# Kernel tuning notes

Hardware: AMD Instinct MI355X
Metric: run time of the kernel (lower is better)

## Reference

```python
import jax, jax.numpy as jnp
import numpy as np
import math

HEADS = 16


def setup_inputs() -> dict:
    key = jax.random.key(0)
    kx, kq, kk, kv = jax.random.split(key, 4)
    B, S, E = 2, 2048, 1024
    x = jax.random.normal(kx, (B, S, E), dtype=jnp.float32)
    # torch nn.Linear weights are [out, in]; y = x @ W.T
    Wq = jax.random.normal(kq, (E, E), dtype=jnp.float32) * (1.0 / math.sqrt(E))
    Wk = jax.random.normal(kk, (E, E), dtype=jnp.float32) * (1.0 / math.sqrt(E))
    Wv = jax.random.normal(kv, (E, E), dtype=jnp.float32) * (1.0 / math.sqrt(E))
    # multiplicative causal mask, as the module applies mask by elementwise multiply
    mask = jnp.tril(jnp.ones((S, S), dtype=jnp.float32))
    return {"x": x, "Wq": Wq, "Wk": Wk, "Wv": Wv, "mask": mask}


def reference(x, Wq, Wk, Wv, mask):
    B, S, E = x.shape
    H = HEADS
    D = E // H
    q = (x @ Wq.T).reshape(B, S, H, D)
    k = (x @ Wk.T).reshape(B, S, H, D)
    v = (x @ Wv.T).reshape(B, S, H, D)
    # scores: [B, H, S, S]
    sim = jnp.einsum('nqhd,nkhd->nhqk', q, k)
    sim = sim * mask  # multiplicative mask, broadcast over (B, H)
    # NOTE: original scales by sqrt(emsize), not sqrt(head_dim)
    attn = jax.nn.softmax(sim / math.sqrt(E), axis=-1)
    out = jnp.einsum('nhql,nlhd->nqhd', attn, v).reshape(B, S, E)
    return out
```

## Files before the change

kernel.cpp:

```cpp
#include <hip/hip_runtime.h>
#include <hip/hip_bf16.h>
#include <cstdint>

using bf16   = __bf16;
using bf16x4 = __attribute__((ext_vector_type(4))) __bf16;
using bf16x8 = __attribute__((ext_vector_type(8))) __bf16;
using f32x4  = __attribute__((ext_vector_type(4))) float;

#define MFMA16(a, b, c) __builtin_amdgcn_mfma_f32_16x16x32_bf16((a), (b), (c), 0, 0, 0)

__device__ __forceinline__ void load_lds16(const bf16* g, bf16* l) {
    __builtin_amdgcn_global_load_lds(
        (const __attribute__((address_space(1))) void*)g,
        (__attribute__((address_space(3))) void*)l, 16, 0, 0);
}

__global__ __launch_bounds__(256) void cast_all(const float* __restrict__ x,
                                                const float* __restrict__ Wq,
                                                const float* __restrict__ Wk,
                                                const float* __restrict__ Wv,
                                                bf16* __restrict__ xb,
                                                bf16* __restrict__ wb,
                                                float qscale) {
    int i = blockIdx.x * 256 + threadIdx.x;
    const float* src; bf16* dst; int off; float scale = 1.0f;
    if (i < 1048576)      { src = x;  dst = xb;              off = i; }
    else if (i < 1310720) { src = Wq; dst = wb;              off = i - 1048576; scale = qscale; }
    else if (i < 1572864) { src = Wk; dst = wb + (1u << 20); off = i - 1310720; }
    else                  { src = Wv; dst = wb + (2u << 20); off = i - 1572864; }
    float4 v = reinterpret_cast<const float4*>(src)[off];
    bf16x4 o;
    o[0] = (bf16)(v.x * scale); o[1] = (bf16)(v.y * scale);
    o[2] = (bf16)(v.z * scale); o[3] = (bf16)(v.w * scale);
    reinterpret_cast<bf16x4*>(dst)[off] = o;
}

__global__ __launch_bounds__(256) void qkv_gemm(const bf16* __restrict__ xb,
                                                const bf16* __restrict__ wb,
                                                bf16* __restrict__ Qo,
                                                bf16* __restrict__ Ko,
                                                bf16* __restrict__ Vt) {
    const int id  = blockIdx.x;
    const int xcd = id & 7;
    const int r   = id >> 3;
    const int ntile = r >> 2;
    const int ms    = r & 3;
    const int mtile = xcd * 4 + ms;
    const int n0 = ntile * 128;
    const int m0 = mtile * 128;

    __shared__ __align__(16) bf16 As[128 * 64];
    __shared__ __align__(16) bf16 Bs[128 * 64];

    const int t    = threadIdx.x;
    const int lane = t & 63;
    const int wid  = t >> 6;
    const int quad = lane >> 4;
    const int col  = lane & 15;
    const int wm   = wid & 1;
    const int wn   = wid >> 1;

    const int rsub = lane >> 3;
    const int csw  = ((lane & 7) ^ rsub) * 8;

    f32x4 acc[4][4] = {};

    const bf16* Ag = &xb[(size_t)(m0 + rsub) * 1024 + csw];
    const bf16* Bg = &wb[(size_t)(n0 + rsub) * 1024 + csw];

    for (int kc = 0; kc < 1024; kc += 64) {
        __syncthreads();
#pragma unroll
        for (int j = 0; j < 4; ++j) {
            const int c = wid * 4 + j;
            load_lds16(Ag + kc + (size_t)c * 8 * 1024, &As[c * 512]);
        }
#pragma unroll
        for (int j = 0; j < 4; ++j) {
            const int c = wid * 4 + j;
            load_lds16(Bg + kc + (size_t)c * 8 * 1024, &Bs[c * 512]);
        }
        __syncthreads();

#pragma unroll
        for (int ks = 0; ks < 2; ++ks) {
            const int ca = ((ks * 4 + quad) ^ (col & 7)) * 8;
            bf16x8 a[4], b[4];
#pragma unroll
            for (int i = 0; i < 4; ++i)
                a[i] = *reinterpret_cast<const bf16x8*>(
                    &As[(wm * 64 + i * 16 + col) * 64 + ca]);
#pragma unroll
            for (int i = 0; i < 4; ++i)
                b[i] = *reinterpret_cast<const bf16x8*>(
                    &Bs[(wn * 64 + i * 16 + col) * 64 + ca]);
#pragma unroll
            for (int mt = 0; mt < 4; ++mt)
#pragma unroll
                for (int nt = 0; nt < 4; ++nt)
                    acc[mt][nt] = MFMA16(a[mt], b[nt], acc[mt][nt]);
        }
    }

    const int w = ntile >> 3;
#pragma unroll
    for (int mt = 0; mt < 4; ++mt) {
#pragma unroll
        for (int nt = 0; nt < 4; ++nt) {
#pragma unroll
            for (int r2 = 0; r2 < 4; ++r2) {
                int m = m0 + wm * 64 + mt * 16 + quad * 4 + r2;
                int n = n0 + wn * 64 + nt * 16 + col;
                int bb = m >> 11, s = m & 2047;
                int n1 = n & 1023;
                int h = n1 >> 6, d = n1 & 63;
                size_t bh = (size_t)(bb * 16 + h);
                bf16 v = (bf16)acc[mt][nt][r2];
                if (w == 0)      Qo[(bh * 2048 + s) * 64 + d] = v;
                else if (w == 1) Ko[(bh * 2048 + s) * 64 + d] = v;
                else             Vt[(bh * 64 + d) * 2048 + s] = v;
            }
        }
    }
}

__global__ __launch_bounds__(256) void tail_kernel(const bf16* __restrict__ Vt,
                                                   float* __restrict__ Tail) {
    const int bh = blockIdx.x >> 3;
    const int dg = blockIdx.x & 7;
    const bf16* Vg = Vt + (size_t)bh * 64 * 2048 + (size_t)dg * 8 * 2048;
    float* Tg = Tail + (size_t)bh * 33 * 64 + dg * 8;

    __shared__ float ts[8 * 33];
    const int tid = threadIdx.x;
    const int d  = tid >> 5;
    const int tt = tid & 31;

    const bf16* p = &Vg[(size_t)d * 2048 + tt * 64];
    float s = 0.0f;
#pragma unroll
    for (int j = 0; j < 8; ++j) {
        bf16x8 v = *reinterpret_cast<const bf16x8*>(p + j * 8);
#pragma unroll
        for (int e = 0; e < 8; ++e) s += (float)v[e];
    }
    ts[d * 33 + tt] = s;
    __syncthreads();

    if (tid < 8) {
        const int dd = tid;
        float acc = 0.0f;
        Tg[32 * 64 + dd] = 0.0f;
        for (int t2 = 31; t2 >= 1; --t2) {
            acc += ts[dd * 33 + t2];
            Tg[t2 * 64 + dd] = acc;
        }
    }
}

__global__ __launch_bounds__(256) void attn_kernel(const bf16* __restrict__ Q,
                                                   const bf16* __restrict__ K,
                                                   const bf16* __restrict__ Vt,
                                                   const float* __restrict__ Tail,
                                                   float* __restrict__ out) {
    const int bid  = blockIdx.x;
    const int work = (bid & 7) * 64 + (bid >> 3);
    const int bh   = work >> 4;
    const int x    = work & 15;
    const int b    = bh >> 4;
    const int h    = bh & 15;

    const int t    = threadIdx.x;
    const int lane = t & 63;
    const int wid  = t >> 6;
    const int quad = lane >> 4;
    const int col  = lane & 15;
    const int qh   = wid & 1;
    const int kh   = wid >> 1;

    const bf16* Qg = Q + (size_t)bh * 2048 * 64;
    const bf16* Kg = K + (size_t)bh * 2048 * 64;
    const bf16* Vg = Vt + (size_t)bh * 64 * 2048;

    __shared__ __align__(16) bf16 Ks[128 * 64];
    __shared__ __align__(16) bf16 Vs[64 * 128];
    __shared__ __align__(16) bf16 Ps[64 * 136];

    bf16x8 ones;
#pragma unroll
    for (int i = 0; i < 8; ++i) ones[i] = (bf16)1.0f;

    const int rsubK = lane >> 3;
    const int cswK  = ((lane & 7) ^ rsubK) * 8;
    const int rV    = lane >> 4;
    const int ccV   = lane & 15;

    for (int pp = 0; pp < 2; ++pp) {
        const int qt = pp == 0 ? (31 - x) : x;
        const int q0 = qt * 64;
        const int np = (qt >> 1) + 1;

        bf16x8 qf[2][2];
#pragma unroll
        for (int qs = 0; qs < 2; ++qs)
#pragma unroll
            for (int ks = 0; ks < 2; ++ks)
                qf[qs][ks] = *reinterpret_cast<const bf16x8*>(
                    &Qg[(size_t)(q0 + qh * 32 + qs * 16 + col) * 64 + ks * 32 + quad * 8]);

        f32x4 o[2][2];
        f32x4 la[2];
        {
            const float tc = 64.0f * (float)(32 - 2 * np);
#pragma unroll
            for (int qs = 0; qs < 2; ++qs)
#pragma unroll
                for (int r = 0; r < 4; ++r) la[qs][r] = tc;
            const float* Tg = Tail + ((size_t)bh * 33 + 2 * np) * 64;
#pragma unroll
            for (int dt = 0; dt < 2; ++dt) {
                float tv = Tg[kh * 32 + dt * 16 + col];
#pragma unroll
                for (int qs = 0; qs < 2; ++qs)
#pragma unroll
                    for (int r = 0; r < 4; ++r) o[qs][dt][r] = tv;
            }
        }

        const int s0max = (np - 1) * 128;

        for (int s0 = 0; s0 < np * 128; s0 += 128) {
            __syncthreads();
#pragma unroll
            for (int jj = 0; jj < 4; ++jj) {
                const int c = wid * 4 + jj;
                load_lds16(&Kg[(size_t)(s0 + c * 8 + rsubK) * 64 + cswK], &Ks[c * 512]);
                const int d = c * 4 + rV;
                load_lds16(&Vg[(size_t)d * 2048 + s0 + ((ccV ^ (d & 15)) * 8)], &Vs[c * 512]);
            }
            __syncthreads();

            f32x4 sv[2][4] = {};
            __builtin_amdgcn_s_setprio(1);
#pragma unroll
            for (int ks = 0; ks < 2; ++ks) {
                const int ca = ((ks * 4 + quad) ^ (col & 7)) * 8;
#pragma unroll
                for (int nt = 0; nt < 4; ++nt) {
                    bf16x8 kb = *reinterpret_cast<const bf16x8*>(
                        &Ks[((kh * 4 + nt) * 16 + col) * 64 + ca]);
                    sv[0][nt] = MFMA16(kb, qf[0][ks], sv[0][nt]);
                    sv[1][nt] = MFMA16(kb, qf[1][ks], sv[1][nt]);
                }
            }
            __builtin_amdgcn_s_setprio(0);

            if (s0 == s0max) {
#pragma unroll
                for (int qs = 0; qs < 2; ++qs) {
                    const int qc = q0 + qh * 32 + qs * 16 + col;
#pragma unroll
                    for (int nt = 0; nt < 4; ++nt)
#pragma unroll
                        for (int r = 0; r < 4; ++r) {
                            int kidx = s0 + kh * 64 + nt * 16 + quad * 4 + r;
                            if (kidx > qc) sv[qs][nt][r] = 0.0f;
                        }
                }
            }

#pragma unroll
            for (int qs = 0; qs < 2; ++qs) {
                bf16* Pq = &Ps[(qh * 32 + qs * 16 + col) * 136 + kh * 64];
#pragma unroll
                for (int nt = 0; nt < 4; ++nt) {
                    bf16x4 pw;
#pragma unroll
                    for (int r = 0; r < 4; ++r)
                        pw[r] = (bf16)__builtin_amdgcn_exp2f(sv[qs][nt][r]);
                    *reinterpret_cast<bf16x4*>(&Pq[nt * 16 + quad * 4]) = pw;
                }
            }

            __syncthreads();

            __builtin_amdgcn_s_setprio(1);
#pragma unroll
            for (int kg = 0; kg < 4; ++kg) {
                bf16x8 pa0 = *reinterpret_cast<const bf16x8*>(
                    &Ps[(qh * 32 + col) * 136 + kg * 32 + quad * 8]);
                bf16x8 pa1 = *reinterpret_cast<const bf16x8*>(
                    &Ps[(qh * 32 + 16 + col) * 136 + kg * 32 + quad * 8]);
                la[0] = MFMA16(pa0, ones, la[0]);
                la[1] = MFMA16(pa1, ones, la[1]);
#pragma unroll
                for (int dt = 0; dt < 2; ++dt) {
                    bf16x8 vb = *reinterpret_cast<const bf16x8*>(
                        &Vs[(kh * 32 + dt * 16 + col) * 128 + ((kg * 4 + quad) ^ col) * 8]);
                    o[0][dt] = MFMA16(pa0, vb, o[0][dt]);
                    o[1][dt] = MFMA16(pa1, vb, o[1][dt]);
                }
            }
            __builtin_amdgcn_s_setprio(0);
        }

#pragma unroll
        for (int qs = 0; qs < 2; ++qs) {
#pragma unroll
            for (int r = 0; r < 4; ++r) {
                int q = q0 + qh * 32 + qs * 16 + quad * 4 + r;
                float inv = __builtin_amdgcn_rcpf(la[qs][r]);
#pragma unroll
                for (int dt = 0; dt < 2; ++dt) {
                    int d = kh * 32 + dt * 16 + col;
                    out[((size_t)b * 2048 + q) * 1024 + h * 64 + d] = o[qs][dt][r] * inv;
                }
            }
        }
    }
}

extern "C" void kernel_launch(void* const* d_in, const int* in_sizes, int n_in,
                              void* d_out, int out_size, void* d_ws, size_t ws_size,
                              hipStream_t stream) {
    const float* x  = (const float*)d_in[0];
    const float* Wq = (const float*)d_in[1];
    const float* Wk = (const float*)d_in[2];
    const float* Wv = (const float*)d_in[3];
    float* out = (float*)d_out;

    char* ws = (char*)d_ws;
    bf16*  xb   = (bf16*)(ws);
    bf16*  wb   = (bf16*)(ws + (size_t)(8  << 20));
    bf16*  Qb   = (bf16*)(ws + (size_t)(14 << 20));
    bf16*  Kb   = (bf16*)(ws + (size_t)(22 << 20));
    bf16*  Vtb  = (bf16*)(ws + (size_t)(30 << 20));
    float* Tail = (float*)(ws + (size_t)(38 << 20));

    const float QSCALE = 1.44269504088896f / 32.0f;

    cast_all<<<7168, 256, 0, stream>>>(x, Wq, Wk, Wv, xb, wb, QSCALE);

    qkv_gemm<<<768, 256, 0, stream>>>(xb, wb, Qb, Kb, Vtb);

    tail_kernel<<<256, 256, 0, stream>>>(Vtb, Tail);

    attn_kernel<<<512, 256, 0, stream>>>(Qb, Kb, Vtb, Tail, out);
}
```

Measured before the change: 157.6 us.

## Prefetch K/V tiles into registers and stage V-transpose stores through LDS

In the attention loop, the next K and V tiles are now loaded from global memory into registers during the PV MFMA phase, then written to LDS at the top of the next iteration. This replaces the direct global-to-LDS loads and is meant to hide global load latency behind compute. In the QKV GEMM, the V-transposed output is first written to shared memory and then stored as coalesced 16-byte rows, replacing scattered 2-byte strided stores. The cost is more register pressure from the prefetch buffers and extra LDS traffic plus synchronisation in the GEMM epilogue.

```diff
diff --git a/kernel.cpp b/kernel.cpp
--- a/kernel.cpp
+++ b/kernel.cpp
@@ -49,8 +49,9 @@
     const int n0 = ntile * 128;
     const int m0 = mtile * 128;
 
-    __shared__ __align__(16) bf16 As[128 * 64];
-    __shared__ __align__(16) bf16 Bs[128 * 64];
+    __shared__ __align__(16) bf16 SM[128 * 132];
+    bf16* const As = SM;
+    bf16* const Bs = SM + 128 * 64;
 
     const int t    = threadIdx.x;
     const int lane = t & 63;
@@ -103,22 +104,48 @@
     }
 
     const int w = ntile >> 3;
-#pragma unroll
-    for (int mt = 0; mt < 4; ++mt) {
-#pragma unroll
-        for (int nt = 0; nt < 4; ++nt) {
-#pragma unroll
-            for (int r2 = 0; r2 < 4; ++r2) {
-                int m = m0 + wm * 64 + mt * 16 + quad * 4 + r2;
-                int n = n0 + wn * 64 + nt * 16 + col;
-                int bb = m >> 11, s = m & 2047;
-                int n1 = n & 1023;
-                int h = n1 >> 6, d = n1 & 63;
-                size_t bh = (size_t)(bb * 16 + h);
-                bf16 v = (bf16)acc[mt][nt][r2];
-                if (w == 0)      Qo[(bh * 2048 + s) * 64 + d] = v;
-                else if (w == 1) Ko[(bh * 2048 + s) * 64 + d] = v;
-                else             Vt[(bh * 64 + d) * 2048 + s] = v;
+    if (w == 2) {
+        __syncthreads();
+#pragma unroll
+        for (int mt = 0; mt < 4; ++mt)
+#pragma unroll
+            for (int nt = 0; nt < 4; ++nt)
+#pragma unroll
+                for (int r2 = 0; r2 < 4; ++r2) {
+                    int s_local = wm * 64 + mt * 16 + quad * 4 + r2;
+                    int n_local = wn * 64 + nt * 16 + col;
+                    SM[n_local * 132 + s_local] = (bf16)acc[mt][nt][r2];
+                }
+        __syncthreads();
+        const int sbase = m0 & 2047;
+        const int bb16  = (m0 >> 11) * 16;
+#pragma unroll
+        for (int i = 0; i < 8; ++i) {
+            int task = i * 256 + t;
+            int row = task >> 4, ch = task & 15;
+            int n1 = (n0 + row) & 1023;
+            int hh = n1 >> 6, dd = n1 & 63;
+            bf16x8 v = *reinterpret_cast<const bf16x8*>(&SM[row * 132 + ch * 8]);
+            *reinterpret_cast<bf16x8*>(
+                &Vt[((size_t)(bb16 + hh) * 64 + dd) * 2048 + sbase + ch * 8]) = v;
+        }
+    } else {
+#pragma unroll
+        for (int mt = 0; mt < 4; ++mt) {
+#pragma unroll
+            for (int nt = 0; nt < 4; ++nt) {
+#pragma unroll
+                for (int r2 = 0; r2 < 4; ++r2) {
+                    int m = m0 + wm * 64 + mt * 16 + quad * 4 + r2;
+                    int n = n0 + wn * 64 + nt * 16 + col;
+                    int bb = m >> 11, s = m & 2047;
+                    int n1 = n & 1023;
+                    int h = n1 >> 6, d = n1 & 63;
+                    size_t bh = (size_t)(bb * 16 + h);
+                    bf16 v = (bf16)acc[mt][nt][r2];
+                    if (w == 0) Qo[(bh * 2048 + s) * 64 + d] = v;
+                    else        Ko[(bh * 2048 + s) * 64 + d] = v;
+                }
             }
         }
     }
@@ -229,14 +256,24 @@
 
         const int s0max = (np - 1) * 128;
 
-        for (int s0 = 0; s0 < np * 128; s0 += 128) {
+        float4 kr[4], vr[4];
+#pragma unroll
+        for (int jj = 0; jj < 4; ++jj) {
+            const int c = wid * 4 + jj;
+            kr[jj] = *reinterpret_cast<const float4*>(
+                &Kg[(size_t)(c * 8 + rsubK) * 64 + cswK]);
+            const int d = c * 4 + rV;
+            vr[jj] = *reinterpret_cast<const float4*>(
+                &Vg[(size_t)d * 2048 + ((ccV ^ (d & 15)) * 8)]);
+        }
+
+        for (int s0 = 0; s0 <= s0max; s0 += 128) {
             __syncthreads();
 #pragma unroll
             for (int jj = 0; jj < 4; ++jj) {
                 const int c = wid * 4 + jj;
-                load_lds16(&Kg[(size_t)(s0 + c * 8 + rsubK) * 64 + cswK], &Ks[c * 512]);
-                const int d = c * 4 + rV;
-                load_lds16(&Vg[(size_t)d * 2048 + s0 + ((ccV ^ (d & 15)) * 8)], &Vs[c * 512]);
+                *reinterpret_cast<float4*>(&Ks[c * 512 + lane * 8]) = kr[jj];
+                *reinterpret_cast<float4*>(&Vs[c * 512 + lane * 8]) = vr[jj];
             }
             __syncthreads();
 
@@ -283,6 +320,19 @@
             }
 
             __syncthreads();
+
+            if (s0 < s0max) {
+                const int s0n = s0 + 128;
+#pragma unroll
+                for (int jj = 0; jj < 4; ++jj) {
+                    const int c = wid * 4 + jj;
+                    kr[jj] = *reinterpret_cast<const float4*>(
+                        &Kg[(size_t)(s0n + c * 8 + rsubK) * 64 + cswK]);
+                    const int d = c * 4 + rV;
+                    vr[jj] = *reinterpret_cast<const float4*>(
+                        &Vg[(size_t)d * 2048 + s0n + ((ccV ^ (d & 15)) * 8)]);
+                }
+            }
 
             __builtin_amdgcn_s_setprio(1);
 #pragma unroll
```

Result: slower. 208.5 us (+32.3%).
